# Optimization experiments

Hardware: AMD Instinct MI355X
Metric: run time of the kernel (lower is better)

Reference implementation:

```python
import jax, jax.numpy as jnp
import numpy as np

IN_FEATURES = 1024
OUT_FEATURES = 256
NUM_KNOTS = 10
SPLINE_ORDER = 3
NUM_BASIS = NUM_KNOTS + SPLINE_ORDER  # 13
EPS = 1e-8


def setup_inputs() -> dict:
    key = jax.random.key(0)
    k1, k2 = jax.random.split(key)
    x = jax.random.normal(k1, (8192, IN_FEATURES), dtype=jnp.float32)
    spline_coeffs = jax.random.normal(
        k2, (OUT_FEATURES, IN_FEATURES, NUM_BASIS), dtype=jnp.float32) * 0.1
    knots = jnp.linspace(-1.0, 1.0, NUM_KNOTS + 2 * SPLINE_ORDER, dtype=jnp.float32)
    return {"x": x, "spline_coeffs": spline_coeffs, "knots": knots}


def _basis_functions(x, knots):
    # x: (B, I) already tanh-normalized; returns (B, I, NUM_BASIS)
    xc = jnp.clip(x, -1.0, 1.0)[..., None]          # (B, I, 1)
    left = knots[:NUM_BASIS - 1]                     # (nb-1,)
    center = knots[1:NUM_BASIS]                      # (nb-1,)
    right = knots[2:NUM_BASIS + 1]                   # (nb-1,)  (i+2 < len(knots) always)
    mask_l = (xc >= left) & (xc < center)
    mask_r = (xc >= center) & (xc < right)
    up = mask_l.astype(xc.dtype) * (xc - left) / (center - left + EPS)
    down = mask_r.astype(xc.dtype) * (right - xc) / (right - center + EPS)
    b = up + down                                    # (B, I, nb-1)
    # last basis column is never written in the original loop -> zeros
    return jnp.pad(b, ((0, 0), (0, 0), (0, 1)))


def reference(x, spline_coeffs, knots):
    x_norm = jnp.tanh(x)
    basis = _basis_functions(x_norm, knots)          # (B, I, K)
    # output[b, j] = sum_i sum_k basis[b, i, k] * coeffs[j, i, k]
    return jnp.einsum('bik,jik->bj', basis, spline_coeffs)
```

## Files before the change

### kernel.cpp

```cpp
#include <hip/hip_runtime.h>
#include <cstdint>
#include <cstddef>


typedef _Float16 half2_v __attribute__((ext_vector_type(2)));
typedef __fp16  fp16x2  __attribute__((ext_vector_type(2)));
typedef _Float16 f16x8 __attribute__((ext_vector_type(8)));
typedef float f32x4 __attribute__((ext_vector_type(4)));

__device__ __forceinline__ half2_v u32_as_h2(uint32_t u) {
  union { uint32_t u; half2_v h; } c; c.u = u; return c.h;
}
__device__ __forceinline__ uint32_t h2_as_u32(half2_v h) {
  union { uint32_t u; half2_v h; } c; c.h = h; return c.u;
}
__device__ __forceinline__ half2_v cvt_pk_h2(float a, float b) {
  union { fp16x2 f; half2_v h; } c;
  c.f = __builtin_amdgcn_cvt_pkrtz(a, b);
  return c.h;
}
__device__ __forceinline__ float dot2f(half2_v a, half2_v b, float c) {
#if __has_builtin(__builtin_amdgcn_fdot2)
  return __builtin_amdgcn_fdot2(a, b, c, false);
#else
  return c + (float)a[0] * (float)b[0] + (float)a[1] * (float)b[1];
#endif
}
__device__ __forceinline__ uint16_t f16_bits(float v) {
  union { _Float16 h; uint16_t u; } c; c.h = (_Float16)v; return c.u;
}

__device__ __forceinline__ float fast_tanhf(float v) {
  const float e = __expf(2.0f * v);
  return 1.0f - 2.0f / (e + 1.0f);
}

#define KSTEP 0.13333333333333333f
#define KINV  7.49999943750004f
__device__ __forceinline__ void kan_weights(float xin, float& w0, float& w1, int& lo) {
  float xc = fast_tanhf(xin);
  xc = fminf(fmaxf(xc, -1.0f), 1.0f);
  int m = (int)((xc + 1.0f) * 7.5f);
  m = min(max(m, 0), 14);
  const float k0 = fmaf((float)m, KSTEP, -1.0f);
  const float up = (xc - k0) * KINV;
  const float dn = (k0 + KSTEP - xc) * KINV;
  w0 = (m == 0) ? up : ((m <= 12) ? dn : 0.0f);
  w1 = (m >= 1 && m <= 11) ? up : 0.0f;
  lo = min(max(m - 1, 0), 11);
}

__device__ __forceinline__ void load_lds16(const void* g, void* l) {
  __builtin_amdgcn_global_load_lds((const __attribute__((address_space(1))) void*)g,
                                   (__attribute__((address_space(3))) void*)l, 16, 0, 0);
}

#define GMM 8192
#define GNN 256
#define KI  16
#define GK2 (1024 * KI)
#define KSPL2 8
#define IPER (1024 / KSPL2)
#define BM2 128
#define BN2 128
#define NIT (IPER / 4)

__global__ __launch_bounds__(256)
void kan_prep_B2(const float* __restrict__ coef, uint32_t* __restrict__ B2) {
  const int tid = blockIdx.x * 256 + threadIdx.x;
  const float* cp = coef + (size_t)tid * 13;
  uint32_t w[8];
#pragma unroll
  for (int q = 0; q < 6; ++q) w[q] = h2_as_u32(cvt_pk_h2(cp[2 * q], cp[2 * q + 1]));
  w[6] = 0u; w[7] = 0u;
  uint4* p = (uint4*)(B2 + (size_t)tid * 8);
  p[0] = make_uint4(w[0], w[1], w[2], w[3]);
  p[1] = make_uint4(w[4], w[5], w[6], w[7]);
}

__global__ __launch_bounds__(256)
void kan_gemm5(const float* __restrict__ x, const _Float16* __restrict__ B2,
               float* __restrict__ out) {
  __shared__ __align__(16) char Bs[2][BN2 * 128];
  __shared__ __align__(16) uint64_t Ws[2][4 * 128];

  const int t    = threadIdx.x;
  const int lane = t & 63;
  const int wv   = t >> 6;
  const int mw   = wv & 1;
  const int nw   = wv >> 1;
  const int fr   = lane & 15;
  const int fq   = lane >> 4;
  const int m0   = blockIdx.x * BM2;
  const int n0   = blockIdx.y * BN2;
  const int i00  = blockIdx.z * IPER;
  const int fb   = (fq & 1) * 2;

  f32x4 acc[4][4];
#pragma unroll
  for (int a = 0; a < 4; ++a)
#pragma unroll
    for (int b = 0; b < 4; ++b) acc[a][b] = (f32x4){0.f, 0.f, 0.f, 0.f};

  const int sn[4] = { (0 * 256 + t) >> 3, (1 * 256 + t) >> 3,
                      (2 * 256 + t) >> 3, (3 * 256 + t) >> 3 };
  const int sc = t & 7;
  const int p_row = t & 127;
  const int p_ip  = (t >> 7) * 2;
  const float* xrow = x + (size_t)(m0 + p_row) * 1024 + p_ip;

  auto stageB = [&](int it) {
    const _Float16* Bb = B2 + (size_t)(i00 + it * 4) * KI;
    char* Bd = (char*)Bs[it & 1];
#pragma unroll
    for (int s = 0; s < 4; ++s) {
      const int c = sc ^ (sn[s] & 7);
      load_lds16(Bb + (size_t)(n0 + sn[s]) * GK2 + c * 8, Bd + (s * 256 + t) * 16);
    }
  };
  auto loadx = [&](int it) -> float2 {
    return *(const float2*)(xrow + i00 + it * 4);
  };
  auto expand = [&](int it, float2 xv) {
    uint64_t* Wd = Ws[it & 1];
#pragma unroll
    for (int d = 0; d < 2; ++d) {
      float w0, w1; int lo;
      kan_weights(d ? xv.y : xv.x, w0, w1, lo);
      const uint32_t wp = (uint32_t)f16_bits(w0) | ((uint32_t)f16_bits(w1) << 16);
      Wd[(p_ip + d) * 128 + p_row] = (uint64_t)wp | ((uint64_t)(uint32_t)lo << 32);
    }
  };

  float2 xc = loadx(0);
  stageB(0);
  expand(0, xc);
  float2 xn = loadx(1);

  for (int it = 0; it < NIT; ++it) {
    __syncthreads();

    if (it + 1 < NIT) {
      stageB(it + 1);
      expand(it + 1, xn);
      if (it + 2 < NIT) xn = loadx(it + 2);
    }

    const char* Bd = (const char*)Bs[it & 1];
    const uint64_t* Wd = Ws[it & 1];
#pragma unroll
    for (int ks = 0; ks < 2; ++ks) {
      const int iloc = ks * 2 + (fq >> 1);
      f16x8 af[4];
#pragma unroll
      for (int mi = 0; mi < 4; ++mi) {
        const uint64_t rec = Wd[iloc * 128 + mw * 64 + mi * 16 + fr];
        const uint32_t wp = (uint32_t)rec;
        const uint32_t lo = (uint32_t)(rec >> 32);
        const int s64 = (int)(lo & 3) * 16;
        const uint64_t lo64 = (uint64_t)wp << s64;
        const uint64_t hi64 = ((lo & 3) == 3) ? (uint64_t)(wp >> 16) : 0ull;
        const uint32_t q0 = lo >> 2;
        const uint64_t wA = ((uint32_t)fb == q0) ? lo64
                            : (((uint32_t)fb == q0 + 1) ? hi64 : 0ull);
        const uint64_t wB = ((uint32_t)(fb + 1) == q0) ? lo64
                            : (((uint32_t)fb == q0) ? hi64 : 0ull);
        union { uint64_t u[2]; f16x8 v; } cv;
        cv.u[0] = wA; cv.u[1] = wB;
        af[mi] = cv.v;
      }
#pragma unroll
      for (int ni = 0; ni < 4; ++ni) {
        const int row = nw * 64 + ni * 16 + fr;
        const int col = ks * 4 + fq;
        const f16x8 bf = *(const f16x8*)(Bd + (row * 8 + (col ^ (row & 7))) * 16);
#pragma unroll
        for (int mi = 0; mi < 4; ++mi)
          acc[mi][ni] = __builtin_amdgcn_mfma_f32_16x16x32_f16(af[mi], bf, acc[mi][ni], 0, 0, 0);
      }
    }
  }

#pragma unroll
  for (int mi = 0; mi < 4; ++mi) {
    const int gr = m0 + mw * 64 + mi * 16 + fq * 4;
#pragma unroll
    for (int ni = 0; ni < 4; ++ni) {
      const int gc = n0 + nw * 64 + ni * 16 + fr;
#pragma unroll
      for (int r = 0; r < 4; ++r)
        atomicAdd(&out[(size_t)(gr + r) * GNN + gc], acc[mi][ni][r]);
    }
  }
}

#define TI 8
#define BT 256
#define JT 32
#define ISPL 2
#define IRANGE (1024 / ISPL)

__global__ __launch_bounds__(256)
void kan_dot2(const float* __restrict__ x, const float* __restrict__ coef,
              float* __restrict__ out) {
  __shared__ uint32_t Plds[TI * 12 * JT];
  const int t    = threadIdx.x;
  const int b    = blockIdx.x * BT + t;
  const int j0   = blockIdx.y * JT;
  const int cbeg = blockIdx.z * (IRANGE / TI);

  float acc[JT];
#pragma unroll
  for (int q = 0; q < JT; ++q) acc[q] = 0.0f;

  const int s_jj   = t & 31;
  const int s_iloc = t >> 5;

  for (int c = cbeg; c < cbeg + IRANGE / TI; ++c) {
    const int i0 = c * TI;
    __syncthreads();
    {
      const float* cp0 = coef + ((size_t)(j0 + s_jj) * 1024 + (i0 + s_iloc)) * 13;
      float cv[13];
#pragma unroll
      for (int s = 0; s < 13; ++s) cv[s] = cp0[s];
#pragma unroll
      for (int r = 0; r < 12; ++r) {
        half2_v h; h[0] = (_Float16)cv[r]; h[1] = (_Float16)cv[r + 1];
        const int slot = ((s_jj >> 2) + r) & 7;
        Plds[(s_iloc * 12 + r) * 32 + slot * 4 + (s_jj & 3)] = h2_as_u32(h);
      }
    }
    uint32_t wr[TI]; int lor[TI];
    {
      const float* xr = x + (size_t)b * 1024 + i0;
      const float4 xa = *(const float4*)(xr);
      const float4 xb = *(const float4*)(xr + 4);
      const float xv[TI] = {xa.x, xa.y, xa.z, xa.w, xb.x, xb.y, xb.z, xb.w};
#pragma unroll
      for (int q = 0; q < TI; ++q) {
        float w0, w1; int lo;
        kan_weights(xv[q], w0, w1, lo);
        wr[q] = (uint32_t)f16_bits(w0) | ((uint32_t)f16_bits(w1) << 16);
        lor[q] = lo;
      }
    }
    __syncthreads();

    const uint4* P4 = (const uint4*)Plds;
#pragma unroll
    for (int ii = 0; ii < TI; ++ii) {
      const half2_v hw = u32_as_h2(wr[ii]);
      const int lo = lor[ii];
      const int base = (ii * 12 + lo) * 8;
#pragma unroll
      for (int g = 0; g < 8; ++g) {
        const uint4 v = P4[base + ((g + lo) & 7)];
        acc[4 * g + 0] = dot2f(hw, u32_as_h2(v.x), acc[4 * g + 0]);
        acc[4 * g + 1] = dot2f(hw, u32_as_h2(v.y), acc[4 * g + 1]);
        acc[4 * g + 2] = dot2f(hw, u32_as_h2(v.z), acc[4 * g + 2]);
        acc[4 * g + 3] = dot2f(hw, u32_as_h2(v.w), acc[4 * g + 3]);
      }
    }
  }

  float* orow = out + (size_t)b * 256 + j0;
#pragma unroll
  for (int q = 0; q < JT; ++q) atomicAdd(orow + q, acc[q]);
}

extern "C" void kernel_launch(void* const* d_in, const int* in_sizes, int n_in,
                              void* d_out, int out_size, void* d_ws, size_t ws_size,
                              hipStream_t stream) {
  const float* x     = (const float*)d_in[0];
  const float* coef  = (const float*)d_in[1];
  float* out = (float*)d_out;

  (void)hipMemsetAsync(out, 0, (size_t)out_size * sizeof(float), stream);

  const size_t nB2 = (size_t)GNN * GK2;
  if (ws_size >= nB2 * 2) {
    _Float16* B2 = (_Float16*)d_ws;
    kan_prep_B2<<<(int)((size_t)GNN * 1024 / 256), 256, 0, stream>>>(coef, (uint32_t*)B2);
    dim3 grid(GMM / BM2, GNN / BN2, KSPL2);
    kan_gemm5<<<grid, 256, 0, stream>>>(x, B2, out);
  } else {
    dim3 grid(8192 / BT, 256 / JT, ISPL);
    kan_dot2<<<grid, 256, 0, stream>>>(x, coef, out);
  }
}
```

Before: 226.6 us.

## Pre-expand sparse A fragments into LDS and halve split-K factor

The expand stage now writes each row's full 16-half basis-weight vector, zero-filled except for the two active entries, into LDS. The MFMA loop can then fetch A fragments with one 16-byte LDS read instead of rebuilding them from a packed record with shifts and selects. This removes ALU work from the inner loop at the cost of more LDS space and store traffic. The split-K factor also drops from 8 to 4, which halves the atomic-add traffic on the output but leaves fewer blocks for parallelism.

Result: faster. 197.3 us (-12.9%).

```diff
diff --git a/kernel.cpp b/kernel.cpp
--- a/kernel.cpp
+++ b/kernel.cpp
@@ -59,7 +59,7 @@
 #define GNN 256
 #define KI  16
 #define GK2 (1024 * KI)
-#define KSPL2 8
+#define KSPL2 4
 #define IPER (1024 / KSPL2)
 #define BM2 128
 #define BN2 128
@@ -79,10 +79,10 @@
 }
 
 __global__ __launch_bounds__(256)
-void kan_gemm5(const float* __restrict__ x, const _Float16* __restrict__ B2,
+void kan_gemm6(const float* __restrict__ x, const _Float16* __restrict__ B2,
                float* __restrict__ out) {
   __shared__ __align__(16) char Bs[2][BN2 * 128];
-  __shared__ __align__(16) uint64_t Ws[2][4 * 128];
+  __shared__ __align__(16) char As[2][4 * 128 * 32];
 
   const int t    = threadIdx.x;
   const int lane = t & 63;
@@ -94,7 +94,6 @@
   const int m0   = blockIdx.x * BM2;
   const int n0   = blockIdx.y * BN2;
   const int i00  = blockIdx.z * IPER;
-  const int fb   = (fq & 1) * 2;
 
   f32x4 acc[4][4];
 #pragma unroll
@@ -122,13 +121,19 @@
     return *(const float2*)(xrow + i00 + it * 4);
   };
   auto expand = [&](int it, float2 xv) {
-    uint64_t* Wd = Ws[it & 1];
+    char* Ab = As[it & 1];
 #pragma unroll
     for (int d = 0; d < 2; ++d) {
       float w0, w1; int lo;
       kan_weights(d ? xv.y : xv.x, w0, w1, lo);
-      const uint32_t wp = (uint32_t)f16_bits(w0) | ((uint32_t)f16_bits(w1) << 16);
-      Wd[(p_ip + d) * 128 + p_row] = (uint64_t)wp | ((uint64_t)(uint32_t)lo << 32);
+      const uint32_t wp  = (uint32_t)f16_bits(w0) | ((uint32_t)f16_bits(w1) << 16);
+      const uint32_t wlo = (lo & 1) ? (wp << 16) : wp;
+      const uint32_t whi = (lo & 1) ? (wp >> 16) : 0u;
+      uint32_t* r = (uint32_t*)(Ab + (size_t)((p_ip + d) * 128 + p_row) * 32);
+      *(uint4*)(r)     = make_uint4(0u, 0u, 0u, 0u);
+      *(uint4*)(r + 4) = make_uint4(0u, 0u, 0u, 0u);
+      r[(lo >> 1) + 1] = whi;
+      r[lo >> 1]       = wlo;
     }
   };
 
@@ -147,28 +152,15 @@
     }
 
     const char* Bd = (const char*)Bs[it & 1];
-    const uint64_t* Wd = Ws[it & 1];
+    const char* Ad = (const char*)As[it & 1];
 #pragma unroll
     for (int ks = 0; ks < 2; ++ks) {
       const int iloc = ks * 2 + (fq >> 1);
       f16x8 af[4];
 #pragma unroll
-      for (int mi = 0; mi < 4; ++mi) {
-        const uint64_t rec = Wd[iloc * 128 + mw * 64 + mi * 16 + fr];
-        const uint32_t wp = (uint32_t)rec;
-        const uint32_t lo = (uint32_t)(rec >> 32);
-        const int s64 = (int)(lo & 3) * 16;
-        const uint64_t lo64 = (uint64_t)wp << s64;
-        const uint64_t hi64 = ((lo & 3) == 3) ? (uint64_t)(wp >> 16) : 0ull;
-        const uint32_t q0 = lo >> 2;
-        const uint64_t wA = ((uint32_t)fb == q0) ? lo64
-                            : (((uint32_t)fb == q0 + 1) ? hi64 : 0ull);
-        const uint64_t wB = ((uint32_t)(fb + 1) == q0) ? lo64
-                            : (((uint32_t)fb == q0) ? hi64 : 0ull);
-        union { uint64_t u[2]; f16x8 v; } cv;
-        cv.u[0] = wA; cv.u[1] = wB;
-        af[mi] = cv.v;
-      }
+      for (int mi = 0; mi < 4; ++mi)
+        af[mi] = *(const f16x8*)(Ad +
+                   ((iloc * 128 + mw * 64 + mi * 16 + fr) * 32 + (fq & 1) * 16));
 #pragma unroll
       for (int ni = 0; ni < 4; ++ni) {
         const int row = nw * 64 + ni * 16 + fr;
@@ -283,7 +275,7 @@
     _Float16* B2 = (_Float16*)d_ws;
     kan_prep_B2<<<(int)((size_t)GNN * 1024 / 256), 256, 0, stream>>>(coef, (uint32_t*)B2);
     dim3 grid(GMM / BM2, GNN / BN2, KSPL2);
-    kan_gemm5<<<grid, 256, 0, stream>>>(x, B2, out);
+    kan_gemm6<<<grid, 256, 0, stream>>>(x, B2, out);
   } else {
     dim3 grid(8192 / BT, 256 / JT, ISPL);
     kan_dot2<<<grid, 256, 0, stream>>>(x, coef, out);
```
